# Optimization experiments

Hardware: AMD Instinct MI355X
Metric: run time of the kernel (lower is better)

Reference implementation:

```python
import jax, jax.numpy as jnp
import numpy as np

WIN, STRIDE = 8, 4          # unfold(-1, 8, 4) in FIDSubsequence.forward
HID, FEAT = 128, 30         # action2motion FID classifier: GRU hidden 128, lin1 -> 30
GAMMA = 1.0                 # SoftDTW default gamma
INF = 1e10


def _windows(xyz):
    x = xyz[0]                                   # (J, 3, T)
    T = x.shape[-1]
    nw = (T - WIN) // STRIDE + 1
    idx = jnp.arange(nw)[:, None] * STRIDE + jnp.arange(WIN)[None, :]
    w = x[:, :, idx]
    seq = w.transpose(3, 2, 0, 1)
    return seq.reshape(WIN, nw, -1)


def _gru_layer(xs, Wih, Whh, bih, bhh):
    # xs: (T, B, in); torch GRU gate order r, z, n
    H = Whh.shape[1]
    def step(h, x):
        gi = x @ Wih.T + bih
        gh = h @ Whh.T + bhh
        ir, iz, i_n = jnp.split(gi, 3, -1)
        hr, hz, h_n = jnp.split(gh, 3, -1)
        r = jax.nn.sigmoid(ir + hr)
        z = jax.nn.sigmoid(iz + hz)
        n = jnp.tanh(i_n + r * h_n)
        h_new = (1.0 - z) * n + z * h
        return h_new, h_new
    h0 = jnp.zeros((xs.shape[1], H), xs.dtype)
    _, hs = jax.lax.scan(step, h0, xs)
    return hs                                    # (T, B, H)


def _feats(xyz, Wih1, Whh1, bih1, bhh1, Wih2, Whh2, bih2, bhh2, W1, b1):
    # Batched equivalent of the per-window classifier loop in distance()
    seq = _windows(xyz)                          # (8, nw, 72)
    h1 = _gru_layer(seq, Wih1, Whh1, bih1, bhh1)
    h2 = _gru_layer(h1, Wih2, Whh2, bih2, bhh2)
    return h2[-1] @ W1.T + b1                    # (nw, 30) -- lengths=8 == full window


def _pairwise_sqdist(f1, f2):
    # ((f1 - f2) ** 2).sum(-1) without materializing (n, m, d)
    d = (f1 * f1).sum(-1)[:, None] + (f2 * f2).sum(-1)[None, :] - 2.0 * (f1 @ f2.T)
    return jnp.maximum(d, 0.0)


def _softdtw(D, gamma):
    # anti-diagonal wavefront: A_k[i] = R[i, k-i]
    n, m = D.shape
    rows = jnp.arange(n)
    def step(carry, k):
        A2, A1 = carry
        j = k - rows
        valid = (j >= 0) & (j < m)
        d = D[rows, jnp.clip(j, 0, m - 1)]
        diag = jnp.concatenate([jnp.where(k == 0, 0.0, INF)[None], A2[:-1]])
        up = jnp.concatenate([jnp.full((1,), INF, D.dtype), A1[:-1]])
        smin = -gamma * jax.nn.logsumexp(-jnp.stack([diag, up, A1]) / gamma, axis=0)
        newA = jnp.where(valid, d + smin, INF)
        return (A1, newA), None
    A = jnp.full((n,), INF, D.dtype)
    (_, last), _ = jax.lax.scan(step, (A, A), jnp.arange(n + m - 1))
    return last[-1]                              # R[n-1, m-1]


def setup_inputs() -> dict:
    key = jax.random.key(0)
    ks = jax.random.split(key, 12)
    T, J, IN = 8196, 24, 72
    s = 1.0 / np.sqrt(HID)
    f32 = jnp.float32
    return {
        "x_xyz": jax.random.normal(ks[0], (1, J, 3, T), f32),
        "y_xyz": jax.random.normal(ks[1], (1, J, 3, T), f32),
        "Wih1": jax.random.uniform(ks[2], (3 * HID, IN), f32, -s, s),
        "Whh1": jax.random.uniform(ks[3], (3 * HID, HID), f32, -s, s),
        "bih1": jax.random.uniform(ks[4], (3 * HID,), f32, -s, s),
        "bhh1": jax.random.uniform(ks[5], (3 * HID,), f32, -s, s),
        "Wih2": jax.random.uniform(ks[6], (3 * HID, HID), f32, -s, s),
        "Whh2": jax.random.uniform(ks[7], (3 * HID, HID), f32, -s, s),
        "bih2": jax.random.uniform(ks[8], (3 * HID,), f32, -s, s),
        "bhh2": jax.random.uniform(ks[9], (3 * HID,), f32, -s, s),
        "W1": jax.random.uniform(ks[10], (FEAT, HID), f32, -s, s),
        "b1": jax.random.uniform(ks[11], (FEAT,), f32, -s, s),
    }


def reference(x_xyz, y_xyz, Wih1, Whh1, bih1, bhh1, Wih2, Whh2, bih2, bhh2, W1, b1):
    f1 = _feats(x_xyz, Wih1, Whh1, bih1, bhh1, Wih2, Whh2, bih2, bhh2, W1, b1)
    f2 = _feats(y_xyz, Wih1, Whh1, bih1, bhh1, Wih2, Whh2, bih2, bhh2, W1, b1)
    D = _pairwise_sqdist(f1, f2)                 # (nw, nw)
    return jnp.reshape(_softdtw(D, GAMMA), (1,))
```

## Files before the change

kernel.cpp:

```cpp
#include <hip/hip_runtime.h>
#include <stdint.h>

#define T_LEN 8196
#define LOG2E 1.4426950408889634f
#define LN2   0.6931471805599453f
#define INF2  1.4426950e10f
#define PD_LD 2080
#define PD_OFF 16

__device__ __forceinline__ float fexp2(float x) {
#if __has_builtin(__builtin_amdgcn_exp2f)
    return __builtin_amdgcn_exp2f(x);
#else
    return __expf(x * LN2);
#endif
}
__device__ __forceinline__ float flog2(float x) {
#if __has_builtin(__builtin_amdgcn_logf)
    return __builtin_amdgcn_logf(x);
#else
    return __logf(x) * LOG2E;
#endif
}
__device__ __forceinline__ float sigm(float x) { return 1.0f / (1.0f + __expf(-x)); }
__device__ __forceinline__ float tanh_f(float x) {
    x = fminf(fmaxf(x, -15.0f), 15.0f);
    float e = __expf(2.0f * x);
    return (e - 1.0f) / (e + 1.0f);
}

__global__ void k_prep(const float* __restrict__ Wih1, const float* __restrict__ Whh1,
                       const float* __restrict__ Wih2, const float* __restrict__ Whh2,
                       float* __restrict__ wt) {
    int gid = blockIdx.x * 256 + threadIdx.x;
    if (gid >= 175104) return;
    const float* src;
    int r, K;
    if (gid < 27648)       { r = gid;          K = 72;  src = Wih1; }
    else if (gid < 76800)  { r = gid - 27648;  K = 128; src = Whh1; }
    else if (gid < 125952) { r = gid - 76800;  K = 128; src = Wih2; }
    else                   { r = gid - 125952; K = 128; src = Whh2; }
    int kc   = r / 1536;
    int rem  = r - kc * 1536;
    int gate = rem >> 9;
    int rem2 = rem & 511;
    int u    = rem2 >> 2;
    int ki   = rem2 & 3;
    wt[gid] = src[(gate * 128 + u) * K + kc * 4 + ki];
}

__global__ __launch_bounds__(256)
void k_gru(const float* __restrict__ X, const float* __restrict__ Y,
           const float* __restrict__ wt,
           const float* __restrict__ bih1, const float* __restrict__ bhh1,
           const float* __restrict__ bih2, const float* __restrict__ bhh2,
           const float* __restrict__ W1, const float* __restrict__ b1,
           float* __restrict__ fbuf) {
    __shared__ __align__(16) float xb[72 * 12];
    __shared__ __align__(16) float h1l[128 * 12];
    __shared__ __align__(16) float h2l[128 * 12];

    const int tid = threadIdx.x;
    const int u = tid & 127;
    const int w0 = (tid >> 7) * 4;
    const int bx = blockIdx.x;
    const int seq = bx >> 8;
    const int wbase = (bx & 255) << 3;
    const float* xp = seq ? Y : X;

    const float* wih1 = wt;
    const float* whh1 = wt + 27648;
    const float* wih2 = wt + 76800;
    const float* whh2 = wt + 125952;
    const int u4 = u << 2;

    const float br1  = bih1[u] + bhh1[u];
    const float bz1  = bih1[128 + u] + bhh1[128 + u];
    const float bni1 = bih1[256 + u];
    const float bnh1 = bhh1[256 + u];
    const float br2  = bih2[u] + bhh2[u];
    const float bz2  = bih2[128 + u] + bhh2[128 + u];
    const float bni2 = bih2[256 + u];
    const float bnh2 = bhh2[256 + u];

    float h1r[4], h2r[4];
#pragma unroll
    for (int j = 0; j < 4; ++j) { h1r[j] = 0.f; h2r[j] = 0.f; }
    for (int e = tid; e < 128 * 12; e += 256) { h1l[e] = 0.f; h2l[e] = 0.f; }
    __syncthreads();

    for (int t = 0; t < 8; ++t) {
        for (int e = tid; e < 72 * 8; e += 256) {
            int k = e >> 3, w = e & 7;
            int jj = k / 3, c = k - jj * 3;
            xb[k * 12 + w] = xp[jj * (3 * T_LEN) + c * T_LEN + ((wbase + w) << 2) + t];
        }
        __syncthreads();

        float ar[4], az[4], ai[4], ah[4];
#pragma unroll
        for (int j = 0; j < 4; ++j) { ar[j] = br1; az[j] = bz1; ai[j] = bni1; ah[j] = bnh1; }
#pragma unroll 1
        for (int kc = 0; kc < 18; ++kc) {
            const float4 wr4 = *(const float4*)&wih1[kc * 1536 + u4];
            const float4 wz4 = *(const float4*)&wih1[kc * 1536 + 512 + u4];
            const float4 wn4 = *(const float4*)&wih1[kc * 1536 + 1024 + u4];
            const float wrk[4] = {wr4.x, wr4.y, wr4.z, wr4.w};
            const float wzk[4] = {wz4.x, wz4.y, wz4.z, wz4.w};
            const float wnk[4] = {wn4.x, wn4.y, wn4.z, wn4.w};
#pragma unroll
            for (int ki = 0; ki < 4; ++ki) {
                const float4 x0 = *(const float4*)&xb[(kc * 4 + ki) * 12 + w0];
                float xv[4] = {x0.x, x0.y, x0.z, x0.w};
#pragma unroll
                for (int j = 0; j < 4; ++j) {
                    ar[j] = fmaf(wrk[ki], xv[j], ar[j]);
                    az[j] = fmaf(wzk[ki], xv[j], az[j]);
                    ai[j] = fmaf(wnk[ki], xv[j], ai[j]);
                }
            }
        }
#pragma unroll 1
        for (int kc = 0; kc < 32; ++kc) {
            const float4 wr4 = *(const float4*)&whh1[kc * 1536 + u4];
            const float4 wz4 = *(const float4*)&whh1[kc * 1536 + 512 + u4];
            const float4 wn4 = *(const float4*)&whh1[kc * 1536 + 1024 + u4];
            const float wrk[4] = {wr4.x, wr4.y, wr4.z, wr4.w};
            const float wzk[4] = {wz4.x, wz4.y, wz4.z, wz4.w};
            const float wnk[4] = {wn4.x, wn4.y, wn4.z, wn4.w};
#pragma unroll
            for (int ki = 0; ki < 4; ++ki) {
                const float4 x0 = *(const float4*)&h1l[(kc * 4 + ki) * 12 + w0];
                float xv[4] = {x0.x, x0.y, x0.z, x0.w};
#pragma unroll
                for (int j = 0; j < 4; ++j) {
                    ar[j] = fmaf(wrk[ki], xv[j], ar[j]);
                    az[j] = fmaf(wzk[ki], xv[j], az[j]);
                    ah[j] = fmaf(wnk[ki], xv[j], ah[j]);
                }
            }
        }
        __syncthreads();
#pragma unroll
        for (int j = 0; j < 4; ++j) {
            float r = sigm(ar[j]);
            float z = sigm(az[j]);
            float n = tanh_f(ai[j] + r * ah[j]);
            h1r[j] = (1.f - z) * n + z * h1r[j];
        }
#pragma unroll
        for (int j = 0; j < 4; ++j) h1l[u * 12 + w0 + j] = h1r[j];
        __syncthreads();

#pragma unroll
        for (int j = 0; j < 4; ++j) { ar[j] = br2; az[j] = bz2; ai[j] = bni2; ah[j] = bnh2; }
#pragma unroll 1
        for (int kc = 0; kc < 32; ++kc) {
            const float4 wr4 = *(const float4*)&wih2[kc * 1536 + u4];
            const float4 wz4 = *(const float4*)&wih2[kc * 1536 + 512 + u4];
            const float4 wn4 = *(const float4*)&wih2[kc * 1536 + 1024 + u4];
            const float wrk[4] = {wr4.x, wr4.y, wr4.z, wr4.w};
            const float wzk[4] = {wz4.x, wz4.y, wz4.z, wz4.w};
            const float wnk[4] = {wn4.x, wn4.y, wn4.z, wn4.w};
#pragma unroll
            for (int ki = 0; ki < 4; ++ki) {
                const float4 x0 = *(const float4*)&h1l[(kc * 4 + ki) * 12 + w0];
                float xv[4] = {x0.x, x0.y, x0.z, x0.w};
#pragma unroll
                for (int j = 0; j < 4; ++j) {
                    ar[j] = fmaf(wrk[ki], xv[j], ar[j]);
                    az[j] = fmaf(wzk[ki], xv[j], az[j]);
                    ai[j] = fmaf(wnk[ki], xv[j], ai[j]);
                }
            }
        }
#pragma unroll 1
        for (int kc = 0; kc < 32; ++kc) {
            const float4 wr4 = *(const float4*)&whh2[kc * 1536 + u4];
            const float4 wz4 = *(const float4*)&whh2[kc * 1536 + 512 + u4];
            const float4 wn4 = *(const float4*)&whh2[kc * 1536 + 1024 + u4];
            const float wrk[4] = {wr4.x, wr4.y, wr4.z, wr4.w};
            const float wzk[4] = {wz4.x, wz4.y, wz4.z, wz4.w};
            const float wnk[4] = {wn4.x, wn4.y, wn4.z, wn4.w};
#pragma unroll
            for (int ki = 0; ki < 4; ++ki) {
                const float4 x0 = *(const float4*)&h2l[(kc * 4 + ki) * 12 + w0];
                float xv[4] = {x0.x, x0.y, x0.z, x0.w};
#pragma unroll
                for (int j = 0; j < 4; ++j) {
                    ar[j] = fmaf(wrk[ki], xv[j], ar[j]);
                    az[j] = fmaf(wzk[ki], xv[j], az[j]);
                    ah[j] = fmaf(wnk[ki], xv[j], ah[j]);
                }
            }
        }
        __syncthreads();
#pragma unroll
        for (int j = 0; j < 4; ++j) {
            float r = sigm(ar[j]);
            float z = sigm(az[j]);
            float n = tanh_f(ai[j] + r * ah[j]);
            h2r[j] = (1.f - z) * n + z * h2r[j];
        }
#pragma unroll
        for (int j = 0; j < 4; ++j) h2l[u * 12 + w0 + j] = h2r[j];
        __syncthreads();
    }

    for (int idx = tid; idx < 8 * 30; idx += 256) {
        int w = idx / 30, ff = idx - w * 30;
        float acc = b1[ff];
        for (int k = 0; k < 128; ++k) acc = fmaf(h2l[k * 12 + w], W1[ff * 128 + k], acc);
        fbuf[(seq * 2048 + wbase + w) * 32 + ff] = acc;
    }
}

__global__ __launch_bounds__(256)
void k_pair(const float* __restrict__ fbuf, float* __restrict__ Ep) {
    __shared__ float f1t[64 * 33];
    __shared__ float f2t[64 * 33];
    const int tid = threadIdx.x;
    const int i0 = blockIdx.y * 64, j0 = blockIdx.x * 64;
    for (int e = tid; e < 64 * 32; e += 256) {
        int r = e >> 5, c = e & 31;
        f1t[r * 33 + c] = fbuf[(i0 + r) * 32 + c];
        f2t[r * 33 + c] = fbuf[(2048 + j0 + r) * 32 + c];
    }
    __syncthreads();
    const int tx = tid & 15, ty = tid >> 4;
    float acc[4][4];
#pragma unroll
    for (int r = 0; r < 4; ++r)
#pragma unroll
        for (int c = 0; c < 4; ++c) acc[r][c] = 0.f;
    for (int k = 0; k < 30; ++k) {
        float a[4], b[4];
#pragma unroll
        for (int r = 0; r < 4; ++r) a[r] = f1t[(ty * 4 + r) * 33 + k];
#pragma unroll
        for (int c = 0; c < 4; ++c) b[c] = f2t[(tx * 4 + c) * 33 + k];
#pragma unroll
        for (int r = 0; r < 4; ++r)
#pragma unroll
            for (int c = 0; c < 4; ++c) {
                float d = a[r] - b[c];
                acc[r][c] = fmaf(d, d, acc[r][c]);
            }
    }
#pragma unroll
    for (int r = 0; r < 4; ++r) {
        float4 v = make_float4(__expf(-acc[r][0]), __expf(-acc[r][1]),
                               __expf(-acc[r][2]), __expf(-acc[r][3]));
        *(float4*)&Ep[(size_t)(i0 + ty * 4 + r) * PD_LD + PD_OFF + j0 + tx * 4] = v;
    }
}

#define DTW_GROUP(G, CT)                                                         \
  {                                                                              \
    float inA, inB, dgl;                                                         \
    if (lane == 0) {                                                             \
        inA = sIn[2 * (G)]; inB = sIn[2 * (G) + 1];                              \
        dgl = ((G) == 0) ? carryA : sIn[2 * (G) - 1];                            \
    } else { inA = pA; inB = pB; dgl = dgPrev; }                                 \
    {                                              \
        float mnG = fminf(fminf(inA, inB), dgl);                                 \
        float lim = mnG + 100.f;                                                 \
        if (Sc > lim) {                                                          \
            int ddg = (int)fmaxf(lim - Sc, -2.0e9f);                             \
            W0 = ldexpf(W0, ddg); W1 = ldexpf(W1, ddg);                          \
            W2 = ldexpf(W2, ddg); W3 = ldexpf(W3, ddg);                          \
            Sc = lim;                                                            \
        }                                                                        \
    }                                                                            \
    float ua = fexp2(Sc - inA);                                                  \
    float ub = fexp2(Sc - inB);                                                  \
    float da = fexp2(Sc - dgl);                                                  \
    float eA0 = CT[0][2*(G)],   eA1 = CT[1][2*(G)];                              \
    float eA2 = CT[2][2*(G)],   eA3 = CT[3][2*(G)];                              \
    float eB0 = CT[0][2*(G)+1], eB1 = CT[1][2*(G)+1];                            \
    float eB2 = CT[2][2*(G)+1], eB3 = CT[3][2*(G)+1];                            \
    float oA0 = eA0 * (da + W0);                                                 \
    float oA1 = eA1 * (W0 + W1);                                                 \
    float oA2 = eA2 * (W1 + W2);                                                 \
    float oA3 = eA3 * (W2 + W3);                                                 \
    float a0 = fmaf(eA0, ua, oA0);                                               \
    float a1 = fmaf(eA1, a0, oA1);                                               \
    float a2 = fmaf(eA2, a1, oA2);                                               \
    float a3 = fmaf(eA3, a2, oA3);                                               \
    float oB0 = eB0 * (ua + a0);                                                 \
    float oB1 = eB1 * (a0 + a1);                                                 \
    float oB2 = eB2 * (a1 + a2);                                                 \
    float oB3 = eB3 * (a2 + a3);                                                 \
    float b0 = fmaf(eB0, ub, oB0);                                               \
    float b1 = fmaf(eB1, b0, oB1);                                               \
    float b2 = fmaf(eB2, b1, oB2);                                               \
    float b3 = fmaf(eB3, b2, oB3);                                               \
    W0 = b0; W1 = b1; W2 = b2; W3 = b3;                                          \
    float blogA = fminf(Sc - flog2(a3), INF2);                                   \
    float blogB = fminf(Sc - flog2(b3), INF2);                                   \
    blog[2 * (G)] = blogA; blog[2 * (G) + 1] = blogB;                            \
    float sA = __shfl_up(blogA, 1);                                              \
    float sB = __shfl_up(blogB, 1);                                              \
    dgPrev = pB; pA = sA; pB = sB;                                               \
    mnAcc = fminf(mnAcc, fminf(sA, sB));                                         \
  }

#define DTW_MACRO(CUR, PF, PVC, PVI, M)                                          \
  {                                                                              \
    const int m = (M);                                                           \
    {       \
        int bs = 8 * (m + 2) - 2 * lane;                                         \
        bs = bs < -16 ? -16 : (bs > 2048 ? 2048 : bs);                           \
        _Pragma("unroll")                                                        \
        for (int r = 0; r < 4; ++r) {                                            \
            _Pragma("unroll")                                                    \
            for (int h = 0; h < 4; ++h) {                                        \
                float2 v = *(const float2*)(rp[r] + bs + 2 * h);                 \
                PF[r][2 * h] = v.x; PF[r][2 * h + 1] = v.y;                      \
            }                                                                    \
        }                                                                        \
    }                                                                            \
    if (b > 0 && lane == 0) {            \
        _Pragma("unroll")                                                        \
        for (int u = 0; u < 8; ++u) {                                            \
            int jc = 8 * (m + 3) + u; jc = jc > 2047 ? 2047 : jc;                \
            PVI[u] = __hip_atomic_load(&bIn[jc], __ATOMIC_RELAXED,               \
                                       __HIP_MEMORY_SCOPE_AGENT);                \
        }                                                                        \
    }                                                                            \
    float blog[8];                                                               \
    float mnAcc = INF2;                                                          \
    DTW_GROUP(0, CUR) DTW_GROUP(1, CUR) DTW_GROUP(2, CUR) DTW_GROUP(3, CUR)      \
    carryA = sIn[7];                                                             \
    if (lane == 63) {                                                            \
        if (b < 7) {                                                             \
            _Pragma("unroll")                                                    \
            for (int c = 0; c < 8; ++c) {                                        \
                int j = 8 * m + c - 126;                                         \
                if (j >= 0 && j < 2048) {                                        \
                    uint64_t pk = ((uint64_t)(uint32_t)j << 32) |                \
                                  (uint64_t)__float_as_uint(blog[c]);            \
                    (void)__hip_atomic_exchange(&bOut[j], pk, __ATOMIC_RELAXED,  \
                                                __HIP_MEMORY_SCOPE_AGENT);       \
                }                                                                \
            }                                                                    \
        } else if (m == 271) {                      \
            res = blog[5];                                                       \
        }                                                                        \
    }                                                                            \
    if (b > 0 && lane == 0) {      \
        bool again = false;                                                      \
        _Pragma("unroll")                                                        \
        for (int u = 0; u < 8; ++u) {                                            \
            int jc = 8 * (m + 1) + u; jc = jc > 2047 ? 2047 : jc;                \
            if ((uint32_t)(PVC[u] >> 32) != (uint32_t)jc) again = true;          \
        }                                                                        \
        while (again) {              \
            __builtin_amdgcn_s_sleep(2);                                         \
            _Pragma("unroll")                                                    \
            for (int u = 0; u < 8; ++u) {                                        \
                int jc = 8 * (m + 1) + u; jc = jc > 2047 ? 2047 : jc;            \
                PVC[u] = __hip_atomic_load(&bIn[jc], __ATOMIC_RELAXED,           \
                                           __HIP_MEMORY_SCOPE_AGENT);            \
            }                                                                    \
            again = false;                                                       \
            _Pragma("unroll")                                                    \
            for (int u = 0; u < 8; ++u) {                                        \
                int jc = 8 * (m + 1) + u; jc = jc > 2047 ? 2047 : jc;            \
                if ((uint32_t)(PVC[u] >> 32) != (uint32_t)jc) again = true;      \
            }                                                                    \
        }                                                                        \
        _Pragma("unroll")                                                        \
        for (int u = 0; u < 8; ++u) sIn[u] = __uint_as_float((uint32_t)PVC[u]);  \
    }                                                                            \
    {                                                          \
        float mn = mnAcc;                                                        \
        if (lane == 0) {                                                         \
            if (b > 0) {                                                         \
                mn = sIn[0];                                                     \
                _Pragma("unroll")                                                \
                for (int c = 1; c < 8; ++c) mn = fminf(mn, sIn[c]);              \
            } else {                                                             \
                mn = INF2;                                                       \
            }                                                                    \
        }                                                                        \
        float wmax = fmaxf(fmaxf(W0, W1), fmaxf(W2, W3));                        \
        float Sc_new;                                                            \
        if (wmax > 0.f) {                                                        \
            int e = (int)((__float_as_uint(wmax) >> 23) & 0xFFu) - 127;          \
            Sc_new = fminf(Sc - (float)e, mn + 100.f);                           \
        } else {                                                                 \
            Sc_new = fminf(mn, 1e9f);                                            \
        }                                                                        \
        int dd = (int)fmaxf(fminf(Sc_new - Sc, 999.f), -999.f);                  \
        W0 = ldexpf(W0, dd); W1 = ldexpf(W1, dd);                                \
        W2 = ldexpf(W2, dd); W3 = ldexpf(W3, dd);                                \
        Sc = Sc_new;                                                             \
    }                                                                            \
  }

__global__ __launch_bounds__(64)
void k_dtw(const float* __restrict__ Ep, uint64_t* bndG, float* __restrict__ out) {
    const int b = blockIdx.x;
    const int lane = threadIdx.x;
    const int r0 = b * 256 + lane * 4;
    const uint64_t* bIn = bndG + (size_t)(b - 1) * 2048;
    uint64_t* bOut = bndG + (size_t)b * 2048;

    const float* rp[4];
#pragma unroll
    for (int r = 0; r < 4; ++r) rp[r] = Ep + (size_t)(r0 + r) * PD_LD + PD_OFF;

    float W0 = 0.f, W1 = 0.f, W2 = 0.f, W3 = 0.f;
    float Sc = 0.f;
    float carryA = (b == 0 && lane == 0) ? 0.f : INF2;
    float res = 0.f;
    float pA = INF2, pB = INF2, dgPrev = INF2;
    float sIn[8];
#pragma unroll
    for (int c = 0; c < 8; ++c) sIn[c] = INF2;

    uint64_t pvs0[8], pvs1[8], pvs2[8];
#pragma unroll
    for (int u = 0; u < 8; ++u) { pvs0[u] = 0; pvs1[u] = 0; pvs2[u] = 0; }

    if (b > 0 && lane == 0) {
        {
            uint64_t p = __hip_atomic_load(&bIn[79], __ATOMIC_RELAXED,
                                           __HIP_MEMORY_SCOPE_AGENT);
            while ((uint32_t)(p >> 32) != 79u) {
                __builtin_amdgcn_s_sleep(8);
                p = __hip_atomic_load(&bIn[79], __ATOMIC_RELAXED,
                                      __HIP_MEMORY_SCOPE_AGENT);
            }
        }
        uint64_t pv[8];
        bool again = true;
        while (again) {
#pragma unroll
            for (int u = 0; u < 8; ++u)
                pv[u] = __hip_atomic_load(&bIn[u], __ATOMIC_RELAXED,
                                          __HIP_MEMORY_SCOPE_AGENT);
            again = false;
#pragma unroll
            for (int u = 0; u < 8; ++u)
                if ((uint32_t)(pv[u] >> 32) != (uint32_t)u) again = true;
            if (again) __builtin_amdgcn_s_sleep(2);
        }
        float mn = INF2;
#pragma unroll
        for (int u = 0; u < 8; ++u) {
            sIn[u] = __uint_as_float((uint32_t)pv[u]);
            mn = fminf(mn, sIn[u]);
        }
        Sc = fminf(mn, 1e9f);
#pragma unroll
        for (int u = 0; u < 8; ++u)
            pvs1[u] = __hip_atomic_load(&bIn[8 + u], __ATOMIC_RELAXED,
                                        __HIP_MEMORY_SCOPE_AGENT);
#pragma unroll
        for (int u = 0; u < 8; ++u)
            pvs2[u] = __hip_atomic_load(&bIn[16 + u], __ATOMIC_RELAXED,
                                        __HIP_MEMORY_SCOPE_AGENT);
    }

    float eT0[4][8], eT1[4][8], eT2[4][8];
#pragma unroll
    for (int tt = 0; tt < 2; ++tt) {
        int bs = 8 * tt - 2 * lane;
        bs = bs < -16 ? -16 : bs;
#pragma unroll
        for (int r = 0; r < 4; ++r) {
            float (*dst)[8] = tt ? eT1 : eT0;
#pragma unroll
            for (int h = 0; h < 4; ++h) {
                float2 v = *(const float2*)(rp[r] + bs + 2 * h);
                dst[r][2 * h] = v.x; dst[r][2 * h + 1] = v.y;
            }
        }
    }

    for (int mm = 0; mm < 273; mm += 3) {
        DTW_MACRO(eT0, eT2, pvs1, pvs0, mm);
        DTW_MACRO(eT1, eT0, pvs2, pvs1, mm + 1);
        DTW_MACRO(eT2, eT1, pvs0, pvs2, mm + 2);
    }

    if (b == 7 && lane == 63) out[0] = res * LN2;
}

extern "C" void kernel_launch(void* const* d_in, const int* in_sizes, int n_in,
                              void* d_out, int out_size, void* d_ws, size_t ws_size,
                              hipStream_t stream) {
    const float* X    = (const float*)d_in[0];
    const float* Y    = (const float*)d_in[1];
    const float* Wih1 = (const float*)d_in[2];
    const float* Whh1 = (const float*)d_in[3];
    const float* bih1 = (const float*)d_in[4];
    const float* bhh1 = (const float*)d_in[5];
    const float* bih2 = (const float*)d_in[8];
    const float* bhh2 = (const float*)d_in[9];
    const float* Wih2 = (const float*)d_in[6];
    const float* Whh2 = (const float*)d_in[7];
    const float* W1   = (const float*)d_in[10];
    const float* b1   = (const float*)d_in[11];
    float* out = (float*)d_out;

    float* ws   = (float*)d_ws;
    float* fbuf = ws;
    uint64_t* bndG = (uint64_t*)(ws + 131072);
    float* Ep   = ws + 131072 + 28672;
    float* wt   = Ep + 4259840 - 175104;

    k_prep<<<684, 256, 0, stream>>>(Wih1, Whh1, Wih2, Whh2, wt);
    k_gru<<<512, 256, 0, stream>>>(X, Y, wt, bih1, bhh1, bih2, bhh2, W1, b1, fbuf);
    k_pair<<<dim3(32, 32), 256, 0, stream>>>(fbuf, Ep);
    k_dtw<<<8, 64, 0, stream>>>(Ep, bndG, out);
}
```

Before: 796.6 us.

## Store exp-distance matrix in DTW tile-major layout and stream tiles via LDS

The pairwise kernel now writes exp(-D) in a skewed, tile-major layout that matches the order in which each DTW lane consumes its anti-diagonal slab. The DTW kernel double-buffers each 2048-float tile into shared memory using global_load_lds direct-to-LDS loads, then reads from LDS instead of issuing strided per-row float2 global loads into rotating register buffers. This targets global load latency on the serial wavefront and cuts register pressure. In exchange it adds a full memset of the enlarged workspace each call, scattered scalar stores in the pair kernel, and a vmcnt(0) wait at every step.

Result: slower. 990.6 us (+24.3%).

```diff
diff --git a/kernel.cpp b/kernel.cpp
--- a/kernel.cpp
+++ b/kernel.cpp
@@ -5,8 +5,8 @@
 #define LOG2E 1.4426950408889634f
 #define LN2   0.6931471805599453f
 #define INF2  1.4426950e10f
-#define PD_LD 2080
-#define PD_OFF 16
+
+#define NTILE 272
 
 __device__ __forceinline__ float fexp2(float x) {
 #if __has_builtin(__builtin_amdgcn_exp2f)
@@ -27,6 +27,11 @@
     x = fminf(fmaxf(x, -15.0f), 15.0f);
     float e = __expf(2.0f * x);
     return (e - 1.0f) / (e + 1.0f);
+}
+__device__ __forceinline__ void gload16(const void* g, void* l) {
+    __builtin_amdgcn_global_load_lds(
+        (const __attribute__((address_space(1))) uint32_t*)g,
+        (__attribute__((address_space(3))) uint32_t*)l, 16, 0, 0);
 }
 
 __global__ void k_prep(const float* __restrict__ Wih1, const float* __restrict__ Whh1,
@@ -249,9 +254,16 @@
     }
 #pragma unroll
     for (int r = 0; r < 4; ++r) {
-        float4 v = make_float4(__expf(-acc[r][0]), __expf(-acc[r][1]),
-                               __expf(-acc[r][2]), __expf(-acc[r][3]));
-        *(float4*)&Ep[(size_t)(i0 + ty * 4 + r) * PD_LD + PD_OFF + j0 + tx * 4] = v;
+        int i = i0 + ty * 4 + r;
+        int b = i >> 8, l = (i >> 2) & 63, rr = i & 3;
+        size_t lb = ((size_t)b * NTILE * 64 + l) * 32 + rr * 8;
+#pragma unroll
+        for (int c = 0; c < 4; ++c) {
+            int j = j0 + tx * 4 + c;
+            int v = j + 2 * l;
+            int m = v >> 3, cc = v & 7;
+            Ep[lb + (size_t)m * 2048 + cc] = __expf(-acc[r][c]);
+        }
     }
 }
 
@@ -305,20 +317,16 @@
     mnAcc = fminf(mnAcc, fminf(sA, sB));                                         \
   }
 
-#define DTW_MACRO(CUR, PF, PVC, PVI, M)                                          \
+#define DTW_MACRO(PVC, PVI, M)                                                   \
   {                                                                              \
     const int m = (M);                                                           \
-    {       \
-        int bs = 8 * (m + 2) - 2 * lane;                                         \
-        bs = bs < -16 ? -16 : (bs > 2048 ? 2048 : bs);                           \
+    asm volatile("s_waitcnt vmcnt(0)" ::: "memory");                             \
+    {          \
+        int mt = m + 1; if (mt > NTILE - 1) mt = NTILE - 1;                      \
+        const float* sb = tb + (size_t)mt * 2048 + lane * 32;                    \
+        float* db = &ldsE[(m + 1) & 1][0];                                       \
         _Pragma("unroll")                                                        \
-        for (int r = 0; r < 4; ++r) {                                            \
-            _Pragma("unroll")                                                    \
-            for (int h = 0; h < 4; ++h) {                                        \
-                float2 v = *(const float2*)(rp[r] + bs + 2 * h);                 \
-                PF[r][2 * h] = v.x; PF[r][2 * h + 1] = v.y;                      \
-            }                                                                    \
-        }                                                                        \
+        for (int h = 0; h < 8; ++h) gload16(sb + h * 4, db + h * 256);           \
     }                                                                            \
     if (b > 0 && lane == 0) {            \
         _Pragma("unroll")                                                        \
@@ -328,9 +336,20 @@
                                        __HIP_MEMORY_SCOPE_AGENT);                \
         }                                                                        \
     }                                                                            \
+    float eT[4][8];                                                              \
+    {                          \
+        const float* cb = &ldsE[m & 1][0];                                       \
+        _Pragma("unroll")                                                        \
+        for (int r = 0; r < 4; ++r) {                                            \
+            float4 lo = *(const float4*)&cb[(2 * r) * 256 + lane * 4];           \
+            float4 hi = *(const float4*)&cb[(2 * r + 1) * 256 + lane * 4];       \
+            eT[r][0]=lo.x; eT[r][1]=lo.y; eT[r][2]=lo.z; eT[r][3]=lo.w;          \
+            eT[r][4]=hi.x; eT[r][5]=hi.y; eT[r][6]=hi.z; eT[r][7]=hi.w;          \
+        }                                                                        \
+    }                                                                            \
     float blog[8];                                                               \
     float mnAcc = INF2;                                                          \
-    DTW_GROUP(0, CUR) DTW_GROUP(1, CUR) DTW_GROUP(2, CUR) DTW_GROUP(3, CUR)      \
+    DTW_GROUP(0, eT) DTW_GROUP(1, eT) DTW_GROUP(2, eT) DTW_GROUP(3, eT)          \
     carryA = sIn[7];                                                             \
     if (lane == 63) {                                                            \
         if (b < 7) {                                                             \
@@ -401,15 +420,13 @@
 
 __global__ __launch_bounds__(64)
 void k_dtw(const float* __restrict__ Ep, uint64_t* bndG, float* __restrict__ out) {
+    __shared__ __align__(16) float ldsE[2][2048];
+
     const int b = blockIdx.x;
     const int lane = threadIdx.x;
-    const int r0 = b * 256 + lane * 4;
     const uint64_t* bIn = bndG + (size_t)(b - 1) * 2048;
     uint64_t* bOut = bndG + (size_t)b * 2048;
-
-    const float* rp[4];
-#pragma unroll
-    for (int r = 0; r < 4; ++r) rp[r] = Ep + (size_t)(r0 + r) * PD_LD + PD_OFF;
+    const float* tb = Ep + (size_t)b * NTILE * 2048;
 
     float W0 = 0.f, W1 = 0.f, W2 = 0.f, W3 = 0.f;
     float Sc = 0.f;
@@ -464,26 +481,17 @@
                                         __HIP_MEMORY_SCOPE_AGENT);
     }
 
-    float eT0[4][8], eT1[4][8], eT2[4][8];
-#pragma unroll
-    for (int tt = 0; tt < 2; ++tt) {
-        int bs = 8 * tt - 2 * lane;
-        bs = bs < -16 ? -16 : bs;
-#pragma unroll
-        for (int r = 0; r < 4; ++r) {
-            float (*dst)[8] = tt ? eT1 : eT0;
-#pragma unroll
-            for (int h = 0; h < 4; ++h) {
-                float2 v = *(const float2*)(rp[r] + bs + 2 * h);
-                dst[r][2 * h] = v.x; dst[r][2 * h + 1] = v.y;
-            }
-        }
+    {
+        const float* sb = tb + lane * 32;
+        float* db = &ldsE[0][0];
+#pragma unroll
+        for (int h = 0; h < 8; ++h) gload16(sb + h * 4, db + h * 256);
     }
 
     for (int mm = 0; mm < 273; mm += 3) {
-        DTW_MACRO(eT0, eT2, pvs1, pvs0, mm);
-        DTW_MACRO(eT1, eT0, pvs2, pvs1, mm + 1);
-        DTW_MACRO(eT2, eT1, pvs0, pvs2, mm + 2);
+        DTW_MACRO(pvs1, pvs0, mm);
+        DTW_MACRO(pvs2, pvs1, mm + 1);
+        DTW_MACRO(pvs0, pvs2, mm + 2);
     }
 
     if (b == 7 && lane == 63) out[0] = res * LN2;
@@ -498,10 +506,10 @@
     const float* Whh1 = (const float*)d_in[3];
     const float* bih1 = (const float*)d_in[4];
     const float* bhh1 = (const float*)d_in[5];
+    const float* Wih2 = (const float*)d_in[6];
+    const float* Whh2 = (const float*)d_in[7];
     const float* bih2 = (const float*)d_in[8];
     const float* bhh2 = (const float*)d_in[9];
-    const float* Wih2 = (const float*)d_in[6];
-    const float* Whh2 = (const float*)d_in[7];
     const float* W1   = (const float*)d_in[10];
     const float* b1   = (const float*)d_in[11];
     float* out = (float*)d_out;
@@ -510,8 +518,9 @@
     float* fbuf = ws;
     uint64_t* bndG = (uint64_t*)(ws + 131072);
     float* Ep   = ws + 131072 + 28672;
-    float* wt   = Ep + 4259840 - 175104;
-
+    float* wt   = Ep + 4456448 - 175104;
+
+    hipMemsetAsync(Ep, 0, (size_t)4456448 * 4, stream);
     k_prep<<<684, 256, 0, stream>>>(Wih1, Whh1, Wih2, Whh2, wt);
     k_gru<<<512, 256, 0, stream>>>(X, Y, wt, bih1, bhh1, bih2, bhh2, W1, b1, fbuf);
     k_pair<<<dim3(32, 32), 256, 0, stream>>>(fbuf, Ep);
```
